# Performance work log

Hardware: AMD Instinct MI355X
Metric: run time of the kernel (lower is better)

Reference implementation:

```python
import jax, jax.numpy as jnp
import numpy as np

B, H, W, C = 2, 64, 64, 256
NH, K = 8, 7
HD = C // NH


def setup_inputs() -> dict:
    key = jax.random.key(0)
    ks = jax.random.split(key, 5)
    s = lambda fan: 1.0 / np.sqrt(fan)
    return {
        "x": jax.random.normal(ks[0], (B, H, W, C), jnp.float32),
        "ln1_w": jnp.ones((C,), jnp.float32),
        "ln1_b": jnp.zeros((C,), jnp.float32),
        "qkv_w": jax.random.normal(ks[1], (3 * C, C), jnp.float32) * s(C),
        "qkv_b": jnp.zeros((3 * C,), jnp.float32),
        "proj_w": jax.random.normal(ks[2], (C, C), jnp.float32) * s(C),
        "proj_b": jnp.zeros((C,), jnp.float32),
        "ln2_w": jnp.ones((C,), jnp.float32),
        "ln2_b": jnp.zeros((C,), jnp.float32),
        "fc1_w": jax.random.normal(ks[3], (4 * C, C), jnp.float32) * s(C),
        "fc1_b": jnp.zeros((4 * C,), jnp.float32),
        "fc2_w": jax.random.normal(ks[4], (C, 4 * C), jnp.float32) * s(4 * C),
        "fc2_b": jnp.zeros((C,), jnp.float32),
    }


def _ln(x, w, b, eps=1e-5):
    m = x.mean(-1, keepdims=True)
    v = ((x - m) ** 2).mean(-1, keepdims=True)
    return (x - m) * jax.lax.rsqrt(v + eps) * w + b


def _nbr_idx(n, k):
    # NATTEN non-causal window: start clamped so the full k-window fits in [0, n)
    half = k // 2
    start = np.clip(np.arange(n) - half, 0, n - k)
    return jnp.asarray(start[:, None] + np.arange(k)[None, :])  # [n, k]


def reference(x, ln1_w, ln1_b, qkv_w, qkv_b, proj_w, proj_b,
              ln2_w, ln2_b, fc1_w, fc1_b, fc2_w, fc2_b):
    shortcut = x
    xn = _ln(x, ln1_w, ln1_b)
    qkv = (xn @ qkv_w.T + qkv_b).reshape(B, H, W, 3, NH, HD)
    qkv = jnp.transpose(qkv, (3, 0, 4, 1, 2, 5))  # [3,B,NH,H,W,HD]
    q, k, v = qkv[0], qkv[1], qkv[2]
    q = q * (HD ** -0.5)
    ih = _nbr_idx(H, K)[:, None, :, None]   # [H,1,K,1]
    iw = _nbr_idx(W, K)[None, :, None, :]   # [1,W,1,K]
    # gather 7x7 neighborhoods -> [B,NH,H,W,K,K,HD] -> [B,NH,H,W,K*K,HD]
    k_nb = k[:, :, ih, iw, :].reshape(B, NH, H, W, K * K, HD)
    v_nb = v[:, :, ih, iw, :].reshape(B, NH, H, W, K * K, HD)
    attn = jnp.einsum("bnijd,bnijkd->bnijk", q, k_nb)  # na2d_qk
    attn = jax.nn.softmax(attn, axis=-1)
    out = jnp.einsum("bnijk,bnijkd->bnijd", attn, v_nb)  # na2d_av
    out = jnp.transpose(out, (0, 2, 3, 1, 4)).reshape(B, H, W, C)
    out = out @ proj_w.T + proj_b
    x = shortcut + out
    h = _ln(x, ln2_w, ln2_b)
    h = jax.nn.gelu(h @ fc1_w.T + fc1_b, approximate=False)
    h = h @ fc2_w.T + fc2_b
    return x + h
```

## Files before the change

### kernel.cpp

```cpp
#include <hip/hip_runtime.h>
#include <math.h>

#define Hdim 64
#define Wdim 64
#define NTOK 8192

typedef unsigned short ushortT;
typedef __attribute__((ext_vector_type(8))) short short8;
typedef __attribute__((ext_vector_type(4))) float floatx4;

__device__ inline ushortT f2bf(float x) {
    union { float f; unsigned u; } v; v.f = x;
    unsigned r = (v.u + 0x7fffu + ((v.u >> 16) & 1u)) >> 16;
    return (ushortT)r;
}

#define GLOAD_LDS16(g, l) __builtin_amdgcn_global_load_lds( \
    (const __attribute__((address_space(1))) unsigned int*)(g), \
    (__attribute__((address_space(3))) unsigned int*)(l), 16, 0, 0)

__global__ __launch_bounds__(256) void prep_kernel(
        const float* __restrict__ qkv_w, const float* __restrict__ proj_w,
        const float* __restrict__ fc1_w, const float* __restrict__ fc2_w,
        ushortT* __restrict__ o_qkv, ushortT* __restrict__ o_proj,
        ushortT* __restrict__ o_fc1, ushortT* __restrict__ o_fc2,
        const float* __restrict__ x, const float* __restrict__ ln1_w,
        const float* __restrict__ ln1_b, ushortT* __restrict__ xn) {
    if (blockIdx.x < 768) {
        int idx = blockIdx.x * 256 + threadIdx.x;
        const float* src; ushortT* dst; int local;
        if (idx < 49152)        { src = qkv_w;  dst = o_qkv;  local = idx; }
        else if (idx < 65536)   { src = proj_w; dst = o_proj; local = idx - 49152; }
        else if (idx < 131072)  { src = fc1_w;  dst = o_fc1;  local = idx - 65536; }
        else                    { src = fc2_w;  dst = o_fc2;  local = idx - 131072; }
        float4 v = ((const float4*)src)[local];
        ushortT o[4] = {f2bf(v.x), f2bf(v.y), f2bf(v.z), f2bf(v.w)};
        *(uint2*)(dst + (size_t)local * 4) = *(uint2*)o;
    } else {
        int wave = threadIdx.x >> 6, lane = threadIdx.x & 63;
        int t = (blockIdx.x - 768) * 4 + wave;
        float4 v = *(const float4*)(x + (size_t)t * 256 + lane * 4);
        float s = v.x + v.y + v.z + v.w;
        float sq = v.x * v.x + v.y * v.y + v.z * v.z + v.w * v.w;
#pragma unroll
        for (int off = 32; off > 0; off >>= 1) {
            s  += __shfl_xor(s, off, 64);
            sq += __shfl_xor(sq, off, 64);
        }
        float mean = s * (1.0f / 256.0f);
        float var  = sq * (1.0f / 256.0f) - mean * mean;
        float r = rsqrtf(var + 1e-5f);
        float4 wv = *(const float4*)(ln1_w + lane * 4);
        float4 bv = *(const float4*)(ln1_b + lane * 4);
        ushortT o[4] = {f2bf((v.x - mean) * r * wv.x + bv.x),
                        f2bf((v.y - mean) * r * wv.y + bv.y),
                        f2bf((v.z - mean) * r * wv.z + bv.z),
                        f2bf((v.w - mean) * r * wv.w + bv.w)};
        *(uint2*)(xn + (size_t)t * 256 + lane * 4) = *(uint2*)o;
    }
}

__global__ __launch_bounds__(256) void ln_v2(const float* __restrict__ x,
                                             const float* __restrict__ w,
                                             const float* __restrict__ b,
                                             ushortT* __restrict__ y) {
    int wave = threadIdx.x >> 6, lane = threadIdx.x & 63;
    int t = blockIdx.x * 4 + wave;
    float4 v = *(const float4*)(x + (size_t)t * 256 + lane * 4);
    float s = v.x + v.y + v.z + v.w;
    float sq = v.x * v.x + v.y * v.y + v.z * v.z + v.w * v.w;
#pragma unroll
    for (int off = 32; off > 0; off >>= 1) {
        s  += __shfl_xor(s, off, 64);
        sq += __shfl_xor(sq, off, 64);
    }
    float mean = s * (1.0f / 256.0f);
    float var  = sq * (1.0f / 256.0f) - mean * mean;
    float r = rsqrtf(var + 1e-5f);
    float4 wv = *(const float4*)(w + lane * 4);
    float4 bv = *(const float4*)(b + lane * 4);
    ushortT o[4] = {f2bf((v.x - mean) * r * wv.x + bv.x),
                    f2bf((v.y - mean) * r * wv.y + bv.y),
                    f2bf((v.z - mean) * r * wv.z + bv.z),
                    f2bf((v.w - mean) * r * wv.w + bv.w)};
    *(uint2*)(y + (size_t)t * 256 + lane * 4) = *(uint2*)o;
}

template <int EPI>
__global__ __launch_bounds__(256) void gemm_bf16_v2(const ushortT* __restrict__ A,
                                                    const ushortT* __restrict__ Bw,
                                                    const float* __restrict__ bias,
                                                    void* __restrict__ out0,
                                                    ushortT* __restrict__ kb,
                                                    ushortT* __restrict__ vb,
                                                    int N, int K) {
    __shared__ ushortT As[64 * 64];
    __shared__ ushortT Bs[64 * 64];
    const int tid  = threadIdx.x;
    const int wave = tid >> 6, lane = tid & 63;
    const int wm = wave >> 1, wn = wave & 1;
    const int ln16 = lane & 15, kg = lane >> 4;
    const int m0 = blockIdx.y * 64, n0 = blockIdx.x * 64;
    const int g8 = (((lane & 7) ^ (lane >> 3)) * 8);
    const int srow = wave * 16 + (lane >> 3);

    const floatx4 fzero = {0.f, 0.f, 0.f, 0.f};
    floatx4 acc[2][2];
#pragma unroll
    for (int i = 0; i < 2; ++i)
#pragma unroll
        for (int j = 0; j < 2; ++j) acc[i][j] = fzero;

    for (int kt = 0; kt < K; kt += 64) {
#pragma unroll
        for (int p = 0; p < 2; ++p) {
            int row = srow + p * 8;
            GLOAD_LDS16(A  + (size_t)(m0 + row) * K + kt + g8, As + wave * 1024 + p * 512);
            GLOAD_LDS16(Bw + (size_t)(n0 + row) * K + kt + g8, Bs + wave * 1024 + p * 512);
        }
        __syncthreads();
#pragma unroll
        for (int s = 0; s < 2; ++s) {
            short8 a[2], b[2];
#pragma unroll
            for (int i = 0; i < 2; ++i) {
                int ra = wm * 32 + i * 16 + ln16;
                a[i] = *(const short8*)(As + ra * 64 + (((s * 4 + kg) ^ (ra & 7)) * 8));
            }
#pragma unroll
            for (int j = 0; j < 2; ++j) {
                int rb = wn * 32 + j * 16 + ln16;
                b[j] = *(const short8*)(Bs + rb * 64 + (((s * 4 + kg) ^ (rb & 7)) * 8));
            }
#pragma unroll
            for (int i = 0; i < 2; ++i)
#pragma unroll
                for (int j = 0; j < 2; ++j)
                    acc[i][j] = __builtin_amdgcn_mfma_f32_16x16x32_bf16(a[i], b[j], acc[i][j], 0, 0, 0);
        }
        __syncthreads();
    }

#pragma unroll
    for (int j = 0; j < 2; ++j) {
        int col = n0 + wn * 32 + j * 16 + ln16;
        float bsv = bias[col];
        if (EPI == 0) {
            int part = col >> 8, h = (col >> 5) & 7, d = col & 31;
            ushortT* dst = part == 0 ? (ushortT*)out0 : (part == 1 ? kb : vb);
            float scl = part == 0 ? 0.17677669529663687f : 1.0f;
#pragma unroll
            for (int i = 0; i < 2; ++i)
#pragma unroll
                for (int r = 0; r < 4; ++r) {
                    int row = m0 + wm * 32 + i * 16 + kg * 4 + r;
                    int bI = row >> 12, tin = row & 4095;
                    dst[((size_t)(bI * 8 + h) * 4096 + tin) * 32 + d] =
                        f2bf((acc[i][j][r] + bsv) * scl);
                }
        } else {
#pragma unroll
            for (int i = 0; i < 2; ++i)
#pragma unroll
                for (int r = 0; r < 4; ++r) {
                    int row = m0 + wm * 32 + i * 16 + kg * 4 + r;
                    float v = acc[i][j][r] + bsv;
                    v = 0.5f * v * (1.0f + erff(v * 0.70710678118654752f));
                    ((ushortT*)out0)[(size_t)row * N + col] = f2bf(v);
                }
        }
    }
}

__global__ __launch_bounds__(256) void gemm_skinny(const ushortT* __restrict__ A,
                                                   const ushortT* __restrict__ Bw,
                                                   const float* __restrict__ bias,
                                                   const float* __restrict__ res,
                                                   float* __restrict__ out,
                                                   int K) {
    __shared__ ushortT As[32 * 64];
    __shared__ ushortT Bs[64 * 64];
    const int tid  = threadIdx.x;
    const int wave = tid >> 6, lane = tid & 63;
    const int wm = wave >> 1, wn = wave & 1;
    const int ln16 = lane & 15, kg = lane >> 4;
    const int m0 = blockIdx.y * 32, n0 = blockIdx.x * 64;
    const int srow = tid >> 3;
    const int spos = tid & 7;
    const int sgc  = spos ^ (srow & 7);
    const int brow = wave * 16 + (lane >> 3);
    const int bg8  = (((lane & 7) ^ (lane >> 3)) * 8);

    const floatx4 fzero = {0.f, 0.f, 0.f, 0.f};
    floatx4 acc[2] = {fzero, fzero};

    for (int kt = 0; kt < K; kt += 64) {
        GLOAD_LDS16(A + (size_t)(m0 + srow) * K + kt + sgc * 8, As + (tid - lane) * 8);
#pragma unroll
        for (int p = 0; p < 2; ++p) {
            int row = brow + p * 8;
            GLOAD_LDS16(Bw + (size_t)(n0 + row) * K + kt + bg8, Bs + wave * 1024 + p * 512);
        }
        __syncthreads();
#pragma unroll
        for (int s = 0; s < 2; ++s) {
            int c = s * 4 + kg;
            int ra = wm * 16 + ln16;
            short8 a = *(const short8*)(As + ra * 64 + ((c ^ (ra & 7)) * 8));
            short8 b[2];
#pragma unroll
            for (int j = 0; j < 2; ++j) {
                int rb = wn * 32 + j * 16 + ln16;
                b[j] = *(const short8*)(Bs + rb * 64 + ((c ^ (rb & 7)) * 8));
            }
            acc[0] = __builtin_amdgcn_mfma_f32_16x16x32_bf16(a, b[0], acc[0], 0, 0, 0);
            acc[1] = __builtin_amdgcn_mfma_f32_16x16x32_bf16(a, b[1], acc[1], 0, 0, 0);
        }
        __syncthreads();
    }

#pragma unroll
    for (int j = 0; j < 2; ++j) {
        int col = n0 + wn * 32 + j * 16 + ln16;
        float bsv = bias[col];
#pragma unroll
        for (int r = 0; r < 4; ++r) {
            int row = m0 + wm * 16 + kg * 4 + r;
            out[(size_t)row * 256 + col] = acc[j][r] + bsv + res[(size_t)row * 256 + col];
        }
    }
}

__global__ __launch_bounds__(256) void natten_v3(const ushortT* __restrict__ qb,
                                                 const ushortT* __restrict__ kb,
                                                 const ushortT* __restrict__ vb,
                                                 ushortT* __restrict__ attn_out) {
    __shared__ ushortT KVs[2 * 196 * 40];
    __shared__ float Ps[64][52];
    ushortT* Ks = KVs;
    ushortT* Vs = KVs + 196 * 40;
    const int tid = threadIdx.x, bid = blockIdx.x;
    const int tile = bid & 63, h = (bid >> 6) & 7, b = bid >> 9;
    const int ti = tile >> 3, tj = tile & 7;
    const int r0 = min(max(ti * 8 - 3, 0), Hdim - 14);
    const int c0 = min(max(tj * 8 - 3, 0), Wdim - 14);
    const size_t base = (size_t)(b * 8 + h) * 4096 * 32;

    for (int idx = tid; idx < 1568; idx += 256) {
        int t = idx;
        const ushortT* src = kb;
        ushortT* dst = Ks;
        if (t >= 784) { t -= 784; src = vb; dst = Vs; }
        int pos = t >> 2, ch = t & 3;
        int dr = pos / 14, dc = pos - dr * 14;
        int tok = (r0 + dr) * 64 + (c0 + dc);
        *(uint4*)(dst + pos * 40 + ch * 8) = *(const uint4*)(src + base + (size_t)tok * 32 + ch * 8);
    }

    const int tl = tid >> 2, s = tid & 3;
    const int i = ti * 8 + (tl >> 3), j = tj * 8 + (tl & 7);
    const int si = min(max(i - 3, 0), Hdim - 7), sj = min(max(j - 3, 0), Wdim - 7);
    const int lbase = (si - r0) * 14 + (sj - c0);
    const int tin = i * 64 + j;

    float q[32];
    {
        const ushortT* qp = qb + base + (size_t)tin * 32;
#pragma unroll
        for (int c4 = 0; c4 < 4; ++c4) {
            uint4 u = *(const uint4*)(qp + c4 * 8);
            unsigned uu[4] = {u.x, u.y, u.z, u.w};
#pragma unroll
            for (int e = 0; e < 4; ++e) {
                union { unsigned v; float f; } lo, hi;
                lo.v = uu[e] << 16; hi.v = uu[e] & 0xffff0000u;
                q[c4 * 8 + e * 2] = lo.f; q[c4 * 8 + e * 2 + 1] = hi.f;
            }
        }
    }
    __syncthreads();

    float sc[13];
#pragma unroll
    for (int cI = 0; cI < 13; ++cI) {
        int n = s + cI * 4;
        if (n < 49) {
            int di = n / 7, dj = n - di * 7;
            const ushortT* kr = Ks + (lbase + di * 14 + dj) * 40;
            float a = 0.f;
#pragma unroll
            for (int c4 = 0; c4 < 4; ++c4) {
                uint4 u = *(const uint4*)(kr + c4 * 8);
                unsigned uu[4] = {u.x, u.y, u.z, u.w};
#pragma unroll
                for (int e = 0; e < 4; ++e) {
                    union { unsigned v; float f; } lo, hi;
                    lo.v = uu[e] << 16; hi.v = uu[e] & 0xffff0000u;
                    a += q[c4 * 8 + e * 2] * lo.f + q[c4 * 8 + e * 2 + 1] * hi.f;
                }
            }
            sc[cI] = a;
        }
    }
    float m = -1e30f;
#pragma unroll
    for (int cI = 0; cI < 13; ++cI) if (s + cI * 4 < 49) m = fmaxf(m, sc[cI]);
    m = fmaxf(m, __shfl_xor(m, 1, 64));
    m = fmaxf(m, __shfl_xor(m, 2, 64));
    float tot = 0.f;
#pragma unroll
    for (int cI = 0; cI < 13; ++cI) if (s + cI * 4 < 49) { sc[cI] = __expf(sc[cI] - m); tot += sc[cI]; }
    tot += __shfl_xor(tot, 1, 64);
    tot += __shfl_xor(tot, 2, 64);
    float inv = 1.0f / tot;
#pragma unroll
    for (int cI = 0; cI < 13; ++cI) if (s + cI * 4 < 49) Ps[tl][s + cI * 4] = sc[cI] * inv;
    __syncthreads();

    float o[8] = {0.f, 0.f, 0.f, 0.f, 0.f, 0.f, 0.f, 0.f};
#pragma unroll
    for (int n = 0; n < 49; ++n) {
        int di = n / 7, dj = n - di * 7;
        float p = Ps[tl][n];
        const ushortT* vr = Vs + (lbase + di * 14 + dj) * 40 + s * 8;
        uint4 u = *(const uint4*)vr;
        unsigned uu[4] = {u.x, u.y, u.z, u.w};
#pragma unroll
        for (int e = 0; e < 4; ++e) {
            union { unsigned v; float f; } lo, hi;
            lo.v = uu[e] << 16; hi.v = uu[e] & 0xffff0000u;
            o[e * 2]     += p * lo.f;
            o[e * 2 + 1] += p * hi.f;
        }
    }
    unsigned up[4];
#pragma unroll
    for (int d = 0; d < 4; ++d)
        up[d] = (unsigned)f2bf(o[2 * d]) | ((unsigned)f2bf(o[2 * d + 1]) << 16);
    size_t tq = (size_t)(b * 4096 + tin);
    *(uint4*)(attn_out + tq * 256 + h * 32 + s * 8) = make_uint4(up[0], up[1], up[2], up[3]);
}

extern "C" void kernel_launch(void* const* d_in, const int* in_sizes, int n_in,
                              void* d_out, int out_size, void* d_ws, size_t ws_size,
                              hipStream_t stream) {
    const float* x      = (const float*)d_in[0];
    const float* ln1_w  = (const float*)d_in[1];
    const float* ln1_b  = (const float*)d_in[2];
    const float* qkv_w  = (const float*)d_in[3];
    const float* qkv_b  = (const float*)d_in[4];
    const float* proj_w = (const float*)d_in[5];
    const float* proj_b = (const float*)d_in[6];
    const float* ln2_w  = (const float*)d_in[7];
    const float* ln2_b  = (const float*)d_in[8];
    const float* fc1_w  = (const float*)d_in[9];
    const float* fc1_b  = (const float*)d_in[10];
    const float* fc2_w  = (const float*)d_in[11];
    const float* fc2_b  = (const float*)d_in[12];
    float* out = (float*)d_out;

    char* ws = (char*)d_ws;
    size_t off = 0;
    ushortT* wqkv = (ushortT*)(ws + off); off += (size_t)196608 * 2;
    ushortT* wproj= (ushortT*)(ws + off); off += (size_t)65536 * 2;
    ushortT* wfc1 = (ushortT*)(ws + off); off += (size_t)262144 * 2;
    ushortT* wfc2 = (ushortT*)(ws + off); off += (size_t)262144 * 2;
    ushortT* xn   = (ushortT*)(ws + off); off += (size_t)NTOK * 256 * 2;
    ushortT* qbuf = (ushortT*)(ws + off); off += (size_t)NTOK * 256 * 2;
    ushortT* kbuf = (ushortT*)(ws + off); off += (size_t)NTOK * 256 * 2;
    ushortT* vbuf = (ushortT*)(ws + off); off += (size_t)NTOK * 256 * 2;
    ushortT* attn = (ushortT*)(ws + off); off += (size_t)NTOK * 256 * 2;
    float*   x2   = (float*)  (ws + off); off += (size_t)NTOK * 256 * 4;
    ushortT* hb   = (ushortT*)(ws + off); off += (size_t)NTOK * 256 * 2;
    ushortT* h1   = (ushortT*)(ws + off); off += (size_t)NTOK * 1024 * 2;

    dim3 blk(256);
    prep_kernel<<<2816, blk, 0, stream>>>(qkv_w, proj_w, fc1_w, fc2_w,
                                          wqkv, wproj, wfc1, wfc2,
                                          x, ln1_w, ln1_b, xn);
    gemm_bf16_v2<0><<<dim3(12, 128), blk, 0, stream>>>(xn, wqkv, qkv_b,
                                                       qbuf, kbuf, vbuf, 768, 256);
    natten_v3<<<1024, blk, 0, stream>>>(qbuf, kbuf, vbuf, attn);
    gemm_skinny<<<dim3(4, 256), blk, 0, stream>>>(attn, wproj, proj_b, x, x2, 256);
    ln_v2<<<2048, blk, 0, stream>>>(x2, ln2_w, ln2_b, hb);
    gemm_bf16_v2<2><<<dim3(16, 128), blk, 0, stream>>>(hb, wfc1, fc1_b,
                                                       h1, nullptr, nullptr, 1024, 256);
    gemm_skinny<<<dim3(4, 256), blk, 0, stream>>>(h1, wfc2, fc2_b, x2, out, 1024);
}
```

Measured before the change: 151.5 us.

## Fuse LayerNorm into the QKV and FC1 GEMM prologues

Each GEMM block now computes LayerNorm for its 64 rows straight from the fp32 input and writes the full 64x256 bf16 A tile into swizzled LDS. Only the weight tiles still stream through the K loop. This removes the separate LN kernels, their launches, and the bf16 xn/hb round-trips through global memory. In exchange, every column block recomputes LN for the same rows (12x for QKV, 16x for FC1) and uses more LDS per block, which may lower occupancy.

```diff
diff --git a/kernel.cpp b/kernel.cpp
--- a/kernel.cpp
+++ b/kernel.cpp
@@ -19,88 +19,63 @@
     (const __attribute__((address_space(1))) unsigned int*)(g), \
     (__attribute__((address_space(3))) unsigned int*)(l), 16, 0, 0)
 
-__global__ __launch_bounds__(256) void prep_kernel(
+__global__ __launch_bounds__(256) void prep_w(
         const float* __restrict__ qkv_w, const float* __restrict__ proj_w,
         const float* __restrict__ fc1_w, const float* __restrict__ fc2_w,
         ushortT* __restrict__ o_qkv, ushortT* __restrict__ o_proj,
-        ushortT* __restrict__ o_fc1, ushortT* __restrict__ o_fc2,
-        const float* __restrict__ x, const float* __restrict__ ln1_w,
-        const float* __restrict__ ln1_b, ushortT* __restrict__ xn) {
-    if (blockIdx.x < 768) {
-        int idx = blockIdx.x * 256 + threadIdx.x;
-        const float* src; ushortT* dst; int local;
-        if (idx < 49152)        { src = qkv_w;  dst = o_qkv;  local = idx; }
-        else if (idx < 65536)   { src = proj_w; dst = o_proj; local = idx - 49152; }
-        else if (idx < 131072)  { src = fc1_w;  dst = o_fc1;  local = idx - 65536; }
-        else                    { src = fc2_w;  dst = o_fc2;  local = idx - 131072; }
-        float4 v = ((const float4*)src)[local];
-        ushortT o[4] = {f2bf(v.x), f2bf(v.y), f2bf(v.z), f2bf(v.w)};
-        *(uint2*)(dst + (size_t)local * 4) = *(uint2*)o;
-    } else {
-        int wave = threadIdx.x >> 6, lane = threadIdx.x & 63;
-        int t = (blockIdx.x - 768) * 4 + wave;
-        float4 v = *(const float4*)(x + (size_t)t * 256 + lane * 4);
-        float s = v.x + v.y + v.z + v.w;
-        float sq = v.x * v.x + v.y * v.y + v.z * v.z + v.w * v.w;
-#pragma unroll
-        for (int off = 32; off > 0; off >>= 1) {
-            s  += __shfl_xor(s, off, 64);
-            sq += __shfl_xor(sq, off, 64);
-        }
-        float mean = s * (1.0f / 256.0f);
-        float var  = sq * (1.0f / 256.0f) - mean * mean;
-        float r = rsqrtf(var + 1e-5f);
-        float4 wv = *(const float4*)(ln1_w + lane * 4);
-        float4 bv = *(const float4*)(ln1_b + lane * 4);
-        ushortT o[4] = {f2bf((v.x - mean) * r * wv.x + bv.x),
-                        f2bf((v.y - mean) * r * wv.y + bv.y),
-                        f2bf((v.z - mean) * r * wv.z + bv.z),
-                        f2bf((v.w - mean) * r * wv.w + bv.w)};
-        *(uint2*)(xn + (size_t)t * 256 + lane * 4) = *(uint2*)o;
-    }
-}
-
-__global__ __launch_bounds__(256) void ln_v2(const float* __restrict__ x,
-                                             const float* __restrict__ w,
-                                             const float* __restrict__ b,
-                                             ushortT* __restrict__ y) {
-    int wave = threadIdx.x >> 6, lane = threadIdx.x & 63;
-    int t = blockIdx.x * 4 + wave;
-    float4 v = *(const float4*)(x + (size_t)t * 256 + lane * 4);
-    float s = v.x + v.y + v.z + v.w;
-    float sq = v.x * v.x + v.y * v.y + v.z * v.z + v.w * v.w;
-#pragma unroll
-    for (int off = 32; off > 0; off >>= 1) {
-        s  += __shfl_xor(s, off, 64);
-        sq += __shfl_xor(sq, off, 64);
-    }
-    float mean = s * (1.0f / 256.0f);
-    float var  = sq * (1.0f / 256.0f) - mean * mean;
-    float r = rsqrtf(var + 1e-5f);
-    float4 wv = *(const float4*)(w + lane * 4);
-    float4 bv = *(const float4*)(b + lane * 4);
-    ushortT o[4] = {f2bf((v.x - mean) * r * wv.x + bv.x),
-                    f2bf((v.y - mean) * r * wv.y + bv.y),
-                    f2bf((v.z - mean) * r * wv.z + bv.z),
-                    f2bf((v.w - mean) * r * wv.w + bv.w)};
-    *(uint2*)(y + (size_t)t * 256 + lane * 4) = *(uint2*)o;
+        ushortT* __restrict__ o_fc1, ushortT* __restrict__ o_fc2) {
+    int idx = blockIdx.x * 256 + threadIdx.x;
+    const float* src; ushortT* dst; int local;
+    if (idx < 49152)        { src = qkv_w;  dst = o_qkv;  local = idx; }
+    else if (idx < 65536)   { src = proj_w; dst = o_proj; local = idx - 49152; }
+    else if (idx < 131072)  { src = fc1_w;  dst = o_fc1;  local = idx - 65536; }
+    else                    { src = fc2_w;  dst = o_fc2;  local = idx - 131072; }
+    float4 v = ((const float4*)src)[local];
+    ushortT o[4] = {f2bf(v.x), f2bf(v.y), f2bf(v.z), f2bf(v.w)};
+    *(uint2*)(dst + (size_t)local * 4) = *(uint2*)o;
 }
 
 template <int EPI>
-__global__ __launch_bounds__(256) void gemm_bf16_v2(const ushortT* __restrict__ A,
-                                                    const ushortT* __restrict__ Bw,
-                                                    const float* __restrict__ bias,
-                                                    void* __restrict__ out0,
-                                                    ushortT* __restrict__ kb,
-                                                    ushortT* __restrict__ vb,
-                                                    int N, int K) {
-    __shared__ ushortT As[64 * 64];
+__global__ __launch_bounds__(256) void gemm_ln_fused(
+        const float* __restrict__ X, const float* __restrict__ lnw,
+        const float* __restrict__ lnb, const ushortT* __restrict__ Bw,
+        const float* __restrict__ bias, void* __restrict__ out0,
+        ushortT* __restrict__ kb, ushortT* __restrict__ vb, int N) {
+    __shared__ ushortT As[64 * 256];
     __shared__ ushortT Bs[64 * 64];
     const int tid  = threadIdx.x;
     const int wave = tid >> 6, lane = tid & 63;
     const int wm = wave >> 1, wn = wave & 1;
     const int ln16 = lane & 15, kg = lane >> 4;
     const int m0 = blockIdx.y * 64, n0 = blockIdx.x * 64;
+
+    {
+        float4 wv = *(const float4*)(lnw + lane * 4);
+        float4 bv = *(const float4*)(lnb + lane * 4);
+        const int c  = lane >> 1;
+        const int hh = (lane & 1) * 4;
+        for (int it = 0; it < 16; ++it) {
+            int row = wave * 16 + it;
+            float4 v = *(const float4*)(X + (size_t)(m0 + row) * 256 + lane * 4);
+            float s  = v.x + v.y + v.z + v.w;
+            float sq = v.x * v.x + v.y * v.y + v.z * v.z + v.w * v.w;
+#pragma unroll
+            for (int off = 32; off > 0; off >>= 1) {
+                s  += __shfl_xor(s, off, 64);
+                sq += __shfl_xor(sq, off, 64);
+            }
+            float mean = s * (1.0f / 256.0f);
+            float var  = sq * (1.0f / 256.0f) - mean * mean;
+            float r = rsqrtf(var + 1e-5f);
+            ushortT o[4] = {f2bf((v.x - mean) * r * wv.x + bv.x),
+                            f2bf((v.y - mean) * r * wv.y + bv.y),
+                            f2bf((v.z - mean) * r * wv.z + bv.z),
+                            f2bf((v.w - mean) * r * wv.w + bv.w)};
+            int pos = (c & 24) | ((c & 7) ^ (row & 7));
+            *(uint2*)(As + row * 256 + pos * 8 + hh) = *(uint2*)o;
+        }
+    }
+
     const int g8 = (((lane & 7) ^ (lane >> 3)) * 8);
     const int srow = wave * 16 + (lane >> 3);
 
@@ -111,26 +86,27 @@
 #pragma unroll
         for (int j = 0; j < 2; ++j) acc[i][j] = fzero;
 
-    for (int kt = 0; kt < K; kt += 64) {
+    for (int kt = 0; kt < 256; kt += 64) {
 #pragma unroll
         for (int p = 0; p < 2; ++p) {
             int row = srow + p * 8;
-            GLOAD_LDS16(A  + (size_t)(m0 + row) * K + kt + g8, As + wave * 1024 + p * 512);
-            GLOAD_LDS16(Bw + (size_t)(n0 + row) * K + kt + g8, Bs + wave * 1024 + p * 512);
+            GLOAD_LDS16(Bw + (size_t)(n0 + row) * 256 + kt + g8, Bs + wave * 1024 + p * 512);
         }
         __syncthreads();
+        const int cb = kt >> 3;
 #pragma unroll
         for (int s = 0; s < 2; ++s) {
+            int cl = s * 4 + kg;
             short8 a[2], b[2];
 #pragma unroll
             for (int i = 0; i < 2; ++i) {
                 int ra = wm * 32 + i * 16 + ln16;
-                a[i] = *(const short8*)(As + ra * 64 + (((s * 4 + kg) ^ (ra & 7)) * 8));
+                a[i] = *(const short8*)(As + ra * 256 + (cb + (cl ^ (ra & 7))) * 8);
             }
 #pragma unroll
             for (int j = 0; j < 2; ++j) {
                 int rb = wn * 32 + j * 16 + ln16;
-                b[j] = *(const short8*)(Bs + rb * 64 + (((s * 4 + kg) ^ (rb & 7)) * 8));
+                b[j] = *(const short8*)(Bs + rb * 64 + ((cl ^ (rb & 7)) * 8));
             }
 #pragma unroll
             for (int i = 0; i < 2; ++i)
@@ -365,25 +341,21 @@
     ushortT* wproj= (ushortT*)(ws + off); off += (size_t)65536 * 2;
     ushortT* wfc1 = (ushortT*)(ws + off); off += (size_t)262144 * 2;
     ushortT* wfc2 = (ushortT*)(ws + off); off += (size_t)262144 * 2;
-    ushortT* xn   = (ushortT*)(ws + off); off += (size_t)NTOK * 256 * 2;
     ushortT* qbuf = (ushortT*)(ws + off); off += (size_t)NTOK * 256 * 2;
     ushortT* kbuf = (ushortT*)(ws + off); off += (size_t)NTOK * 256 * 2;
     ushortT* vbuf = (ushortT*)(ws + off); off += (size_t)NTOK * 256 * 2;
     ushortT* attn = (ushortT*)(ws + off); off += (size_t)NTOK * 256 * 2;
     float*   x2   = (float*)  (ws + off); off += (size_t)NTOK * 256 * 4;
-    ushortT* hb   = (ushortT*)(ws + off); off += (size_t)NTOK * 256 * 2;
     ushortT* h1   = (ushortT*)(ws + off); off += (size_t)NTOK * 1024 * 2;
 
     dim3 blk(256);
-    prep_kernel<<<2816, blk, 0, stream>>>(qkv_w, proj_w, fc1_w, fc2_w,
-                                          wqkv, wproj, wfc1, wfc2,
-                                          x, ln1_w, ln1_b, xn);
-    gemm_bf16_v2<0><<<dim3(12, 128), blk, 0, stream>>>(xn, wqkv, qkv_b,
-                                                       qbuf, kbuf, vbuf, 768, 256);
+    prep_w<<<768, blk, 0, stream>>>(qkv_w, proj_w, fc1_w, fc2_w,
+                                    wqkv, wproj, wfc1, wfc2);
+    gemm_ln_fused<0><<<dim3(12, 128), blk, 0, stream>>>(x, ln1_w, ln1_b, wqkv, qkv_b,
+                                                        qbuf, kbuf, vbuf, 768);
     natten_v3<<<1024, blk, 0, stream>>>(qbuf, kbuf, vbuf, attn);
     gemm_skinny<<<dim3(4, 256), blk, 0, stream>>>(attn, wproj, proj_b, x, x2, 256);
-    ln_v2<<<2048, blk, 0, stream>>>(x2, ln2_w, ln2_b, hb);
-    gemm_bf16_v2<2><<<dim3(16, 128), blk, 0, stream>>>(hb, wfc1, fc1_b,
-                                                       h1, nullptr, nullptr, 1024, 256);
+    gemm_ln_fused<2><<<dim3(16, 128), blk, 0, stream>>>(x2, ln2_w, ln2_b, wfc1, fc1_b,
+                                                        h1, nullptr, nullptr, 1024);
     gemm_skinny<<<dim3(4, 256), blk, 0, stream>>>(h1, wfc2, fc2_b, x2, out, 1024);
 }
```

Measured after the change: 186.5 us. 23.1% more time.
